# Kernel optimization log

Measured on AMD Instinct MI355X. Metric: run time of the kernel, lower is better.

Reference implementation:

```python
import jax, jax.numpy as jnp
import numpy as np

N0, N1, N2, N3 = 1000000, 102400, 10240, 1024
E0, E1, E2 = 1024000, 102400, 10240
D_IN, D_H, D_OUT = 128, 256, 40


def setup_inputs() -> dict:
    key = jax.random.key(0)
    ks = jax.random.split(key, 16)
    return {
        "x": jax.random.normal(ks[0], (N0, D_IN), jnp.float32),
        "src0": jax.random.randint(ks[1], (E0,), 0, N0, jnp.int32),
        "dst0": jax.random.randint(ks[2], (E0,), 0, N1, jnp.int32),
        "src1": jax.random.randint(ks[3], (E1,), 0, N1, jnp.int32),
        "dst1": jax.random.randint(ks[4], (E1,), 0, N2, jnp.int32),
        "src2": jax.random.randint(ks[5], (E2,), 0, N2, jnp.int32),
        "dst2": jax.random.randint(ks[6], (E2,), 0, N3, jnp.int32),
        "Wl0": jax.random.normal(ks[7], (D_IN, D_H), jnp.float32) / np.sqrt(D_IN),
        "bl0": jnp.zeros((D_H,), jnp.float32),
        "Wr0": jax.random.normal(ks[8], (D_IN, D_H), jnp.float32) / np.sqrt(D_IN),
        "Wl1": jax.random.normal(ks[9], (D_H, D_H), jnp.float32) / np.sqrt(D_H),
        "bl1": jnp.zeros((D_H,), jnp.float32),
        "Wr1": jax.random.normal(ks[10], (D_H, D_H), jnp.float32) / np.sqrt(D_H),
        "Wl2": jax.random.normal(ks[11], (D_H, D_OUT), jnp.float32) / np.sqrt(D_H),
        "bl2": jnp.zeros((D_OUT,), jnp.float32),
        "Wr2": jax.random.normal(ks[12], (D_H, D_OUT), jnp.float32) / np.sqrt(D_H),
    }


def _sage_conv(h, src, dst, n_tgt, Wl, bl, Wr):
    # PyG SAGEConv (mean aggr): out = lin_l(mean_{j in N(i)} h_j) + lin_r(h_i)
    h_tgt = h[:n_tgt]
    msg = h[src]                                               # gather [E, d]
    s = jax.ops.segment_sum(msg, dst, num_segments=n_tgt)       # scatter-add
    cnt = jax.ops.segment_sum(jnp.ones((src.shape[0],), h.dtype), dst,
                              num_segments=n_tgt)
    aggr = s / jnp.maximum(cnt, 1.0)[:, None]
    return aggr @ Wl + bl + h_tgt @ Wr


def reference(x, src0, dst0, src1, dst1, src2, dst2,
              Wl0, bl0, Wr0, Wl1, bl1, Wr1, Wl2, bl2, Wr2):
    h = jax.nn.relu(_sage_conv(x, src0, dst0, N1, Wl0, bl0, Wr0))
    # dropout p=0.5 is identity in eval mode
    h = jax.nn.relu(_sage_conv(h, src1, dst1, N2, Wl1, bl1, Wr1))
    h = _sage_conv(h, src2, dst2, N3, Wl2, bl2, Wr2)
    return jax.nn.log_softmax(h, axis=-1)
```

## Files before the change

### kernel.cpp

```cpp
#include <hip/hip_runtime.h>
#include <hip/hip_bf16.h>

#define N0 1000000
#define N1 102400
#define N2 10240
#define N3 1024
#define E0 1024000
#define E1 102400
#define E2 10240
#define D_IN 128
#define D_H 256
#define D_OUT 40

#define NTOT (N1 + N2 + N3)
#define ETOT (E0 + E1 + E2)

typedef float f4 __attribute__((ext_vector_type(4)));
typedef float f2 __attribute__((ext_vector_type(2)));


__global__ void zero_ints(int* __restrict__ p, int n) {
    int i = blockIdx.x * blockDim.x + threadIdx.x;
    if (i < n) p[i] = 0;
}

__global__ void count_deg_all(const int* __restrict__ d0, const int* __restrict__ d1,
                              const int* __restrict__ d2, int* __restrict__ deg) {
    int e = blockIdx.x * blockDim.x + threadIdx.x;
    if (e < E0)            atomicAdd(&deg[d0[e]], 1);
    else if (e < E0 + E1)  atomicAdd(&deg[N1 + d1[e - E0]], 1);
    else if (e < ETOT)     atomicAdd(&deg[N1 + N2 + d2[e - E0 - E1]], 1);
}

__global__ __launch_bounds__(256)
void scan_blocks(const int* __restrict__ deg, int n,
                 int* __restrict__ rs, int* __restrict__ bsum) {
    __shared__ int s[256];
    int b = blockIdx.x, t = threadIdx.x;
    int base = b * 1024 + t * 4;
    int v[4]; int sum = 0;
    #pragma unroll
    for (int k = 0; k < 4; ++k) {
        int idx = base + k;
        v[k] = (idx < n) ? deg[idx] : 0;
        sum += v[k];
    }
    s[t] = sum; __syncthreads();
    for (int off = 1; off < 256; off <<= 1) {
        int x = (t >= off) ? s[t - off] : 0;
        __syncthreads();
        s[t] += x;
        __syncthreads();
    }
    int excl = s[t] - sum;
    #pragma unroll
    for (int k = 0; k < 4; ++k) {
        int idx = base + k;
        if (idx < n) rs[idx] = excl;
        excl += v[k];
    }
    if (t == 255) bsum[b] = s[255];
}

__global__ __launch_bounds__(256)
void scan_top(int* __restrict__ bsum, int nb) {
    __shared__ int s[256];
    int t = threadIdx.x;
    int v = (t < nb) ? bsum[t] : 0;
    s[t] = v; __syncthreads();
    for (int off = 1; off < 256; off <<= 1) {
        int x = (t >= off) ? s[t - off] : 0;
        __syncthreads();
        s[t] += x;
        __syncthreads();
    }
    if (t < nb) bsum[t] = s[t] - v;
}

__global__ void add_offsets(int* __restrict__ rs, int n, const int* __restrict__ bsum) {
    int i = blockIdx.x * blockDim.x + threadIdx.x;
    if (i < n) rs[i] += bsum[i >> 10];
}

__global__ void fill_edges_all(const int* __restrict__ s0, const int* __restrict__ d0,
                               const int* __restrict__ s1, const int* __restrict__ d1,
                               const int* __restrict__ s2, const int* __restrict__ d2,
                               int* __restrict__ rs, int* __restrict__ esrc) {
    int e = blockIdx.x * blockDim.x + threadIdx.x;
    int sv, gr;
    if (e < E0)           { sv = s0[e];           gr = d0[e]; }
    else if (e < E0 + E1) { sv = s1[e - E0];      gr = N1 + d1[e - E0]; }
    else if (e < ETOT)    { sv = s2[e - E0 - E1]; gr = N1 + N2 + d2[e - E0 - E1]; }
    else return;
    int pos = atomicAdd(&rs[gr], 1);
    esrc[pos] = sv;
}

template<int D>
__global__ __launch_bounds__(256)
void gather_mean(const float* __restrict__ h, const int* __restrict__ rs_after,
                 const int* __restrict__ esrc, float* __restrict__ aggr,
                 int M, int has_prev) {
    int row  = blockIdx.x * (blockDim.x >> 6) + (threadIdx.x >> 6);
    int lane = threadIdx.x & 63;
    if (row >= M) return;
    int start = (row > 0) ? rs_after[row - 1] : (has_prev ? rs_after[-1] : 0);
    int end   = rs_after[row];
    constexpr int F = D / 128;
    f2 acc[F] = {};
    int j = start;
    for (; j + 1 < end; j += 2) {
        int s0 = esrc[j], s1 = esrc[j + 1];
        const f2* p0 = (const f2*)(h + (size_t)s0 * D) + lane;
        const f2* p1 = (const f2*)(h + (size_t)s1 * D) + lane;
        #pragma unroll
        for (int f = 0; f < F; ++f) acc[f] += p0[f * 64] + p1[f * 64];
    }
    if (j < end) {
        int s0 = esrc[j];
        const f2* p0 = (const f2*)(h + (size_t)s0 * D) + lane;
        #pragma unroll
        for (int f = 0; f < F; ++f) acc[f] += p0[f * 64];
    }
    float inv = 1.0f / fmaxf((float)(end - start), 1.0f);
    f2* o = (f2*)(aggr + (size_t)row * D) + lane;
    #pragma unroll
    for (int f = 0; f < F; ++f) o[f * 64] = acc[f] * inv;
}

template<int BM, bool RELU>
__global__ __launch_bounds__(256, 4)
void sage_gemm_v2(const float* __restrict__ A0,
                  const float* __restrict__ A1,
                  const float* __restrict__ B0,
                  const float* __restrict__ B1,
                  const float* __restrict__ bias,
                  float* __restrict__ out,
                  int M, int N, int K) {
    constexpr int BK = 32;
    constexpr int BN = 128;
    constexpr int MH = BM / 64;

    __shared__ float As[BK][BM + 4];
    __shared__ float Bs[BK][BN];

    const int t   = threadIdx.x;
    const int tx4 = (t & 15) << 2;
    const int ty4 = (t >> 4) << 2;
    const int row0 = blockIdx.y * BM;
    const int col0 = blockIdx.x * BN;

    float acc[MH][4][2][4] = {};

    for (int half = 0; half < 2; ++half) {
        const float* __restrict__ Ap = half ? A1 : A0;
        const float* __restrict__ Bp = half ? B1 : B0;
        for (int k0 = 0; k0 < K; k0 += BK) {
            #pragma unroll
            for (int l = 0; l < BM / 32; ++l) {
                int fidx = l * 256 + t;
                int m  = fidx >> 3;
                int kq = (fidx & 7) << 2;
                f4 v = *(const f4*)&Ap[(size_t)(row0 + m) * K + k0 + kq];
                #pragma unroll
                for (int j = 0; j < 4; ++j) As[kq + j][m] = v[j];
            }
            #pragma unroll
            for (int l = 0; l < 4; ++l) {
                int fidx = l * 256 + t;
                int kk = fidx >> 5;
                int c  = (fidx & 31) << 2;
                *(f4*)&Bs[kk][c] = *(const f4*)&Bp[(size_t)(k0 + kk) * N + col0 + c];
            }
            __syncthreads();

            #pragma unroll
            for (int kk = 0; kk < BK; ++kk) {
                f4 a[MH], b[2];
                #pragma unroll
                for (int h = 0; h < MH; ++h)
                    a[h] = *(const f4*)&As[kk][h * 64 + ty4];
                b[0] = *(const f4*)&Bs[kk][tx4];
                b[1] = *(const f4*)&Bs[kk][tx4 + 64];
                #pragma unroll
                for (int h = 0; h < MH; ++h)
                    #pragma unroll
                    for (int i = 0; i < 4; ++i)
                        #pragma unroll
                        for (int n = 0; n < 2; ++n)
                            #pragma unroll
                            for (int j = 0; j < 4; ++j)
                                acc[h][i][n][j] += a[h][i] * b[n][j];
            }
            __syncthreads();
        }
    }

    f4 bv0 = *(const f4*)&bias[col0 + tx4];
    f4 bv1 = *(const f4*)&bias[col0 + tx4 + 64];
    #pragma unroll
    for (int h = 0; h < MH; ++h) {
        #pragma unroll
        for (int i = 0; i < 4; ++i) {
            int r = row0 + h * 64 + ty4 + i;
            f4 v0, v1;
            #pragma unroll
            for (int j = 0; j < 4; ++j) {
                v0[j] = acc[h][i][0][j] + bv0[j];
                v1[j] = acc[h][i][1][j] + bv1[j];
                if (RELU) { v0[j] = fmaxf(v0[j], 0.f); v1[j] = fmaxf(v1[j], 0.f); }
            }
            *(f4*)&out[(size_t)r * N + col0 + tx4]      = v0;
            *(f4*)&out[(size_t)r * N + col0 + tx4 + 64] = v1;
        }
    }
}

__global__ __launch_bounds__(256)
void sage_l2_softmax(const float* __restrict__ aggr,
                     const float* __restrict__ htgt,
                     const float* __restrict__ Wl,
                     const float* __restrict__ Wr,
                     const float* __restrict__ bias,
                     float* __restrict__ out) {
    __shared__ float Bs[D_H * D_OUT];
    const int t = threadIdx.x;
    const int wave = t >> 6, lane = t & 63;
    const int row = blockIdx.x * 4 + wave;

    float a[4], h[4];
    #pragma unroll
    for (int q = 0; q < 4; ++q) {
        a[q] = aggr[(size_t)row * D_H + q * 64 + lane];
        h[q] = htgt[(size_t)row * D_H + q * 64 + lane];
    }
    const int jc = (lane < D_OUT) ? lane : 0;
    float acc = 0.f;
    constexpr int NF = (D_H * D_OUT) / 4;

    {
        const f4* w4 = (const f4*)Wl;
        f4* bs4 = (f4*)Bs;
        for (int i = t; i < NF; i += 256) bs4[i] = w4[i];
    }
    __syncthreads();
    #pragma unroll
    for (int q = 0; q < 4; ++q)
        for (int kk = 0; kk < 64; ++kk)
            acc += __shfl(a[q], kk, 64) * Bs[(q * 64 + kk) * D_OUT + jc];
    __syncthreads();

    {
        const f4* w4 = (const f4*)Wr;
        f4* bs4 = (f4*)Bs;
        for (int i = t; i < NF; i += 256) bs4[i] = w4[i];
    }
    __syncthreads();
    #pragma unroll
    for (int q = 0; q < 4; ++q)
        for (int kk = 0; kk < 64; ++kk)
            acc += __shfl(h[q], kk, 64) * Bs[(q * 64 + kk) * D_OUT + jc];

    float val = (lane < D_OUT) ? acc + bias[jc] : -INFINITY;
    float m = val;
    #pragma unroll
    for (int off = 32; off; off >>= 1) m = fmaxf(m, __shfl_xor(m, off, 64));
    float e = (lane < D_OUT) ? expf(val - m) : 0.f;
    float s = e;
    #pragma unroll
    for (int off = 32; off; off >>= 1) s += __shfl_xor(s, off, 64);
    if (lane < D_OUT) out[(size_t)row * D_OUT + lane] = val - m - logf(s);
}

extern "C" void kernel_launch(void* const* d_in, const int* in_sizes, int n_in,
                              void* d_out, int out_size, void* d_ws, size_t ws_size,
                              hipStream_t stream) {
    const float* x    = (const float*)d_in[0];
    const int*   src0 = (const int*)d_in[1];
    const int*   dst0 = (const int*)d_in[2];
    const int*   src1 = (const int*)d_in[3];
    const int*   dst1 = (const int*)d_in[4];
    const int*   src2 = (const int*)d_in[5];
    const int*   dst2 = (const int*)d_in[6];
    const float* Wl0  = (const float*)d_in[7];
    const float* bl0  = (const float*)d_in[8];
    const float* Wr0  = (const float*)d_in[9];
    const float* Wl1  = (const float*)d_in[10];
    const float* bl1  = (const float*)d_in[11];
    const float* Wr1  = (const float*)d_in[12];
    const float* Wl2  = (const float*)d_in[13];
    const float* bl2  = (const float*)d_in[14];
    const float* Wr2  = (const float*)d_in[15];
    float* out = (float*)d_out;
    float* f   = (float*)d_ws;

    float* h1    = f;
    float* aggr0 = f + (size_t)26214400;
    float* aggr1 = f + (size_t)26214400;
    float* h2    = f + (size_t)28835840;
    float* aggr2 = f + (size_t)31457280;
    int* ib   = (int*)(f + (size_t)39321600);
    int* esrc = ib;
    int* deg  = ib + ETOT;
    int* rs   = ib + ETOT + NTOT;
    int* bsum = ib + ETOT + 2 * NTOT;

    zero_ints<<<(NTOT + 255) / 256, 256, 0, stream>>>(deg, NTOT);
    count_deg_all<<<(ETOT + 255) / 256, 256, 0, stream>>>(dst0, dst1, dst2, deg);
    int nb = (NTOT + 1023) / 1024;
    scan_blocks<<<nb, 256, 0, stream>>>(deg, NTOT, rs, bsum);
    scan_top<<<1, 256, 0, stream>>>(bsum, nb);
    add_offsets<<<(NTOT + 255) / 256, 256, 0, stream>>>(rs, NTOT, bsum);
    fill_edges_all<<<(ETOT + 255) / 256, 256, 0, stream>>>(
        src0, dst0, src1, dst1, src2, dst2, rs, esrc);

    gather_mean<D_IN><<<N1 / 4, 256, 0, stream>>>(x, rs, esrc, aggr0, N1, 0);
    sage_gemm_v2<128, true><<<dim3(D_H / 128, N1 / 128), 256, 0, stream>>>(
        aggr0, x, Wl0, Wr0, bl0, h1, N1, D_H, D_IN);

    gather_mean<D_H><<<N2 / 4, 256, 0, stream>>>(h1, rs + N1, esrc, aggr1, N2, 1);
    sage_gemm_v2<64, true><<<dim3(D_H / 128, N2 / 64), 256, 0, stream>>>(
        aggr1, h1, Wl1, Wr1, bl1, h2, N2, D_H, D_H);

    gather_mean<D_H><<<N3 / 4, 256, 0, stream>>>(h2, rs + N1 + N2, esrc, aggr2, N3, 1);
    sage_l2_softmax<<<N3 / 4, 256, 0, stream>>>(aggr2, h2, Wl2, Wr2, bl2, out);
}
```

Measured before the change: 1.161 ms.

## Use bf16 MFMA GEMMs and bf16 intermediates for first two SAGE layers

Replaces the FP32 SIMT tiled GEMM with a bf16 MFMA kernel (16x16x32) and adds a prep kernel that transposes the layer-0/1 weights and converts them to bf16. The aggregates and the h1 activations are stored in bf16, which halves the gather and GEMM memory traffic. The gather loop in layer 0 is also unrolled by 4 to keep more loads in flight. Accuracy drops to bf16 precision, and the weight conversion now runs on every call.

```diff
diff --git a/kernel.cpp b/kernel.cpp
--- a/kernel.cpp
+++ b/kernel.cpp
@@ -17,7 +17,19 @@
 
 typedef float f4 __attribute__((ext_vector_type(4)));
 typedef float f2 __attribute__((ext_vector_type(2)));
-
+typedef unsigned short u16x8 __attribute__((ext_vector_type(8)));
+typedef unsigned short u16x4 __attribute__((ext_vector_type(4)));
+typedef short s16x8 __attribute__((ext_vector_type(8)));
+
+static __device__ __forceinline__ unsigned short f2b(float x) {
+    union { float f; unsigned u; } c; c.f = x;
+    unsigned r = c.u + 0x7FFF + ((c.u >> 16) & 1);
+    return (unsigned short)(r >> 16);
+}
+static __device__ __forceinline__ float b2f(unsigned short u) {
+    union { unsigned u; float f; } c; c.u = (unsigned)u << 16;
+    return c.f;
+}
 
 __global__ void zero_ints(int* __restrict__ p, int n) {
     int i = blockIdx.x * blockDim.x + threadIdx.x;
@@ -96,122 +108,182 @@
     esrc[pos] = sv;
 }
 
-template<int D>
-__global__ __launch_bounds__(256)
-void gather_mean(const float* __restrict__ h, const int* __restrict__ rs_after,
-                 const int* __restrict__ esrc, float* __restrict__ aggr,
-                 int M, int has_prev) {
+__global__ __launch_bounds__(256)
+void prep_weights(const float* __restrict__ Wl0, const float* __restrict__ Wr0,
+                  const float* __restrict__ Wl1, const float* __restrict__ Wr1,
+                  unsigned short* __restrict__ Wt0l, unsigned short* __restrict__ Wt0r,
+                  unsigned short* __restrict__ Wt1l, unsigned short* __restrict__ Wt1r) {
+    int i = blockIdx.x * 256 + threadIdx.x;
+    if (i < D_IN * D_H) {
+        int k = i >> 8, n = i & 255;
+        Wt0l[n * D_IN + k] = f2b(Wl0[i]);
+        Wt0r[n * D_IN + k] = f2b(Wr0[i]);
+    }
+    if (i < D_H * D_H) {
+        int k = i >> 8, n = i & 255;
+        Wt1l[n * D_H + k] = f2b(Wl1[i]);
+        Wt1r[n * D_H + k] = f2b(Wr1[i]);
+    }
+}
+
+__global__ __launch_bounds__(256)
+void gather_mean_f32_bf16(const float* __restrict__ h, const int* __restrict__ rs_after,
+                          const int* __restrict__ esrc, unsigned* __restrict__ aggr,
+                          int M) {
     int row  = blockIdx.x * (blockDim.x >> 6) + (threadIdx.x >> 6);
     int lane = threadIdx.x & 63;
     if (row >= M) return;
-    int start = (row > 0) ? rs_after[row - 1] : (has_prev ? rs_after[-1] : 0);
+    int start = (row > 0) ? rs_after[row - 1] : 0;
     int end   = rs_after[row];
-    constexpr int F = D / 128;
-    f2 acc[F] = {};
+    f2 acc = {0.f, 0.f};
     int j = start;
-    for (; j + 1 < end; j += 2) {
-        int s0 = esrc[j], s1 = esrc[j + 1];
-        const f2* p0 = (const f2*)(h + (size_t)s0 * D) + lane;
-        const f2* p1 = (const f2*)(h + (size_t)s1 * D) + lane;
+    for (; j + 3 < end; j += 4) {
+        int s0 = esrc[j], s1 = esrc[j + 1], s2 = esrc[j + 2], s3 = esrc[j + 3];
+        acc += ((const f2*)(h + (size_t)s0 * D_IN))[lane];
+        acc += ((const f2*)(h + (size_t)s1 * D_IN))[lane];
+        acc += ((const f2*)(h + (size_t)s2 * D_IN))[lane];
+        acc += ((const f2*)(h + (size_t)s3 * D_IN))[lane];
+    }
+    for (; j < end; ++j)
+        acc += ((const f2*)(h + (size_t)esrc[j] * D_IN))[lane];
+    float inv = 1.0f / fmaxf((float)(end - start), 1.0f);
+    unsigned pack = (unsigned)f2b(acc.x * inv) | ((unsigned)f2b(acc.y * inv) << 16);
+    aggr[(size_t)row * 64 + lane] = pack;
+}
+
+__global__ __launch_bounds__(256)
+void gather_mean_bf16(const unsigned short* __restrict__ h, const int* __restrict__ rs_after,
+                      const int* __restrict__ esrc, unsigned short* __restrict__ aggr,
+                      int M) {
+    int row  = blockIdx.x * (blockDim.x >> 6) + (threadIdx.x >> 6);
+    int lane = threadIdx.x & 63;
+    if (row >= M) return;
+    int start = (row > 0) ? rs_after[row - 1] : rs_after[-1];
+    int end   = rs_after[row];
+    float acc[4] = {};
+    for (int j = start; j < end; ++j) {
+        const u16x4 v = *(const u16x4*)(h + (size_t)esrc[j] * D_H + lane * 4);
         #pragma unroll
-        for (int f = 0; f < F; ++f) acc[f] += p0[f * 64] + p1[f * 64];
-    }
-    if (j < end) {
-        int s0 = esrc[j];
-        const f2* p0 = (const f2*)(h + (size_t)s0 * D) + lane;
-        #pragma unroll
-        for (int f = 0; f < F; ++f) acc[f] += p0[f * 64];
+        for (int q = 0; q < 4; ++q) acc[q] += b2f(v[q]);
     }
     float inv = 1.0f / fmaxf((float)(end - start), 1.0f);
-    f2* o = (f2*)(aggr + (size_t)row * D) + lane;
-    #pragma unroll
-    for (int f = 0; f < F; ++f) o[f * 64] = acc[f] * inv;
-}
-
-template<int BM, bool RELU>
-__global__ __launch_bounds__(256, 4)
-void sage_gemm_v2(const float* __restrict__ A0,
-                  const float* __restrict__ A1,
-                  const float* __restrict__ B0,
-                  const float* __restrict__ B1,
-                  const float* __restrict__ bias,
-                  float* __restrict__ out,
-                  int M, int N, int K) {
-    constexpr int BK = 32;
-    constexpr int BN = 128;
-    constexpr int MH = BM / 64;
-
-    __shared__ float As[BK][BM + 4];
-    __shared__ float Bs[BK][BN];
-
-    const int t   = threadIdx.x;
-    const int tx4 = (t & 15) << 2;
-    const int ty4 = (t >> 4) << 2;
-    const int row0 = blockIdx.y * BM;
-    const int col0 = blockIdx.x * BN;
-
-    float acc[MH][4][2][4] = {};
-
+    u16x4 o;
+    #pragma unroll
+    for (int q = 0; q < 4; ++q) o[q] = f2b(acc[q] * inv);
+    *(u16x4*)(aggr + (size_t)row * D_H + lane * 4) = o;
+}
+
+__global__ __launch_bounds__(256)
+void gather_mean_f32(const float* __restrict__ h, const int* __restrict__ rs_after,
+                     const int* __restrict__ esrc, float* __restrict__ aggr, int M) {
+    int row  = blockIdx.x * (blockDim.x >> 6) + (threadIdx.x >> 6);
+    int lane = threadIdx.x & 63;
+    if (row >= M) return;
+    int start = (row > 0) ? rs_after[row - 1] : rs_after[-1];
+    int end   = rs_after[row];
+    f2 acc[2] = {};
+    for (int j = start; j < end; ++j) {
+        const f2* p = (const f2*)(h + (size_t)esrc[j] * D_H) + lane;
+        acc[0] += p[0];
+        acc[1] += p[64];
+    }
+    float inv = 1.0f / fmaxf((float)(end - start), 1.0f);
+    f2* o = (f2*)(aggr + (size_t)row * D_H) + lane;
+    o[0]  = acc[0] * inv;
+    o[64] = acc[1] * inv;
+}
+
+template<bool A1F32, bool RELU, bool OUTBF16>
+__global__ __launch_bounds__(256)
+void sage_gemm_mfma(const unsigned short* __restrict__ A0,
+                    const void* __restrict__ A1,
+                    const unsigned short* __restrict__ Bl,
+                    const unsigned short* __restrict__ Br,
+                    const float* __restrict__ bias,
+                    void* __restrict__ out,
+                    int M, int K) {
+    __shared__ unsigned short As[64][40];
+    __shared__ unsigned short Bs[256][40];
+
+    const int t = threadIdx.x;
+    const int lane = t & 63;
+    const int w = t >> 6;
+    const int row0 = blockIdx.x * 64;
+
+    const int lrow = lane & 15;
+    const int kq   = (lane >> 4) * 8;
+
+    f4 acc[4][4] = {};
+
+    const int ar = t >> 2;
+    const int ac = (t & 3) * 8;
+
+    #pragma unroll
     for (int half = 0; half < 2; ++half) {
-        const float* __restrict__ Ap = half ? A1 : A0;
-        const float* __restrict__ Bp = half ? B1 : B0;
-        for (int k0 = 0; k0 < K; k0 += BK) {
-            #pragma unroll
-            for (int l = 0; l < BM / 32; ++l) {
-                int fidx = l * 256 + t;
-                int m  = fidx >> 3;
-                int kq = (fidx & 7) << 2;
-                f4 v = *(const f4*)&Ap[(size_t)(row0 + m) * K + k0 + kq];
-                #pragma unroll
-                for (int j = 0; j < 4; ++j) As[kq + j][m] = v[j];
+        const unsigned short* __restrict__ Bp = half ? Br : Bl;
+        for (int k0 = 0; k0 < K; k0 += 32) {
+            {
+                size_t gidx = (size_t)(row0 + ar) * K + k0 + ac;
+                u16x8 v;
+                if (half == 0) {
+                    v = *(const u16x8*)(A0 + gidx);
+                } else if (!A1F32) {
+                    v = *(const u16x8*)((const unsigned short*)A1 + gidx);
+                } else {
+                    const float* p = (const float*)A1 + gidx;
+                    f4 x0 = *(const f4*)p;
+                    f4 x1 = *(const f4*)(p + 4);
+                    v[0] = f2b(x0[0]); v[1] = f2b(x0[1]); v[2] = f2b(x0[2]); v[3] = f2b(x0[3]);
+                    v[4] = f2b(x1[0]); v[5] = f2b(x1[1]); v[6] = f2b(x1[2]); v[7] = f2b(x1[3]);
+                }
+                *(u16x8*)&As[ar][ac] = v;
             }
             #pragma unroll
-            for (int l = 0; l < 4; ++l) {
-                int fidx = l * 256 + t;
-                int kk = fidx >> 5;
-                int c  = (fidx & 31) << 2;
-                *(f4*)&Bs[kk][c] = *(const f4*)&Bp[(size_t)(k0 + kk) * N + col0 + c];
+            for (int i = 0; i < 4; ++i) {
+                int idx = i * 256 + t;
+                int n = idx >> 2, c = (idx & 3) * 8;
+                *(u16x8*)&Bs[n][c] = *(const u16x8*)(Bp + (size_t)n * K + k0 + c);
             }
             __syncthreads();
 
+            s16x8 a[4], b[4];
             #pragma unroll
-            for (int kk = 0; kk < BK; ++kk) {
-                f4 a[MH], b[2];
+            for (int mf = 0; mf < 4; ++mf)
+                a[mf] = *(const s16x8*)&As[mf * 16 + lrow][kq];
+            #pragma unroll
+            for (int nf = 0; nf < 4; ++nf)
+                b[nf] = *(const s16x8*)&Bs[w * 64 + nf * 16 + lrow][kq];
+            #pragma unroll
+            for (int mf = 0; mf < 4; ++mf)
                 #pragma unroll
-                for (int h = 0; h < MH; ++h)
-                    a[h] = *(const f4*)&As[kk][h * 64 + ty4];
-                b[0] = *(const f4*)&Bs[kk][tx4];
-                b[1] = *(const f4*)&Bs[kk][tx4 + 64];
-                #pragma unroll
-                for (int h = 0; h < MH; ++h)
-                    #pragma unroll
-                    for (int i = 0; i < 4; ++i)
-                        #pragma unroll
-                        for (int n = 0; n < 2; ++n)
-                            #pragma unroll
-                            for (int j = 0; j < 4; ++j)
-                                acc[h][i][n][j] += a[h][i] * b[n][j];
-            }
+                for (int nf = 0; nf < 4; ++nf)
+                    acc[mf][nf] = __builtin_amdgcn_mfma_f32_16x16x32_bf16(
+                        a[mf], b[nf], acc[mf][nf], 0, 0, 0);
             __syncthreads();
         }
     }
 
-    f4 bv0 = *(const f4*)&bias[col0 + tx4];
-    f4 bv1 = *(const f4*)&bias[col0 + tx4 + 64];
-    #pragma unroll
-    for (int h = 0; h < MH; ++h) {
+    const int crow = (lane >> 4) * 4;
+    const int ccol = lane & 15;
+    float bv[4];
+    #pragma unroll
+    for (int nf = 0; nf < 4; ++nf) bv[nf] = bias[w * 64 + nf * 16 + ccol];
+
+    #pragma unroll
+    for (int mf = 0; mf < 4; ++mf) {
         #pragma unroll
-        for (int i = 0; i < 4; ++i) {
-            int r = row0 + h * 64 + ty4 + i;
-            f4 v0, v1;
+        for (int nf = 0; nf < 4; ++nf) {
+            int c = w * 64 + nf * 16 + ccol;
             #pragma unroll
-            for (int j = 0; j < 4; ++j) {
-                v0[j] = acc[h][i][0][j] + bv0[j];
-                v1[j] = acc[h][i][1][j] + bv1[j];
-                if (RELU) { v0[j] = fmaxf(v0[j], 0.f); v1[j] = fmaxf(v1[j], 0.f); }
+            for (int rg = 0; rg < 4; ++rg) {
+                int r = row0 + mf * 16 + crow + rg;
+                float v = acc[mf][nf][rg] + bv[nf];
+                if (RELU) v = fmaxf(v, 0.f);
+                if (OUTBF16)
+                    ((unsigned short*)out)[(size_t)r * 256 + c] = f2b(v);
+                else
+                    ((float*)out)[(size_t)r * 256 + c] = v;
             }
-            *(f4*)&out[(size_t)r * N + col0 + tx4]      = v0;
-            *(f4*)&out[(size_t)r * N + col0 + tx4 + 64] = v1;
         }
     }
 }
@@ -294,16 +366,22 @@
     float* out = (float*)d_out;
     float* f   = (float*)d_ws;
 
-    float* h1    = f;
-    float* aggr0 = f + (size_t)26214400;
-    float* aggr1 = f + (size_t)26214400;
-    float* h2    = f + (size_t)28835840;
-    float* aggr2 = f + (size_t)31457280;
-    int* ib   = (int*)(f + (size_t)39321600);
+    unsigned short* h1b    = (unsigned short*)f;
+    unsigned short* aggr0b = (unsigned short*)(f + (size_t)13107200);
+    unsigned short* aggr1b = (unsigned short*)(f + (size_t)19660800);
+    float* h2    = f + (size_t)20971520;
+    float* aggr2 = f + (size_t)23592960;
+    unsigned short* Wt0l = (unsigned short*)(f + (size_t)23855104);
+    unsigned short* Wt0r = Wt0l + 32768;
+    unsigned short* Wt1l = Wt0r + 32768;
+    unsigned short* Wt1r = Wt1l + 65536;
+    int* ib   = (int*)(f + (size_t)23953408);
     int* esrc = ib;
     int* deg  = ib + ETOT;
     int* rs   = ib + ETOT + NTOT;
     int* bsum = ib + ETOT + 2 * NTOT;
+
+    prep_weights<<<256, 256, 0, stream>>>(Wl0, Wr0, Wl1, Wr1, Wt0l, Wt0r, Wt1l, Wt1r);
 
     zero_ints<<<(NTOT + 255) / 256, 256, 0, stream>>>(deg, NTOT);
     count_deg_all<<<(ETOT + 255) / 256, 256, 0, stream>>>(dst0, dst1, dst2, deg);
@@ -314,14 +392,14 @@
     fill_edges_all<<<(ETOT + 255) / 256, 256, 0, stream>>>(
         src0, dst0, src1, dst1, src2, dst2, rs, esrc);
 
-    gather_mean<D_IN><<<N1 / 4, 256, 0, stream>>>(x, rs, esrc, aggr0, N1, 0);
-    sage_gemm_v2<128, true><<<dim3(D_H / 128, N1 / 128), 256, 0, stream>>>(
-        aggr0, x, Wl0, Wr0, bl0, h1, N1, D_H, D_IN);
-
-    gather_mean<D_H><<<N2 / 4, 256, 0, stream>>>(h1, rs + N1, esrc, aggr1, N2, 1);
-    sage_gemm_v2<64, true><<<dim3(D_H / 128, N2 / 64), 256, 0, stream>>>(
-        aggr1, h1, Wl1, Wr1, bl1, h2, N2, D_H, D_H);
-
-    gather_mean<D_H><<<N3 / 4, 256, 0, stream>>>(h2, rs + N1 + N2, esrc, aggr2, N3, 1);
+    gather_mean_f32_bf16<<<N1 / 4, 256, 0, stream>>>(x, rs, esrc, (unsigned*)aggr0b, N1);
+    sage_gemm_mfma<true, true, true><<<N1 / 64, 256, 0, stream>>>(
+        aggr0b, x, Wt0l, Wt0r, bl0, h1b, N1, D_IN);
+
+    gather_mean_bf16<<<N2 / 4, 256, 0, stream>>>(h1b, rs + N1, esrc, aggr1b, N2);
+    sage_gemm_mfma<false, true, false><<<N2 / 64, 256, 0, stream>>>(
+        aggr1b, h1b, Wt1l, Wt1r, bl1, h2, N2, D_H);
+
+    gather_mean_f32<<<N3 / 4, 256, 0, stream>>>(h2, rs + N1 + N2, esrc, aggr2, N3);
     sage_l2_softmax<<<N3 / 4, 256, 0, stream>>>(aggr2, h2, Wl2, Wr2, bl2, out);
 }
```

Result: faster. 968.2 us (-16.6%).
